# Kernel tuning notes

Hardware: AMD Instinct MI355X
Metric: run time of the kernel (lower is better)

Reference implementation:

```python
import jax, jax.numpy as jnp
import numpy as np

EPS = 1e-7
N_CAPS_J = 24
ROUTE_MIN = 0.0
N_ITER = 3
INV_TEMP = 0.5
INV_TEMP_DELTA = 0.1


def create_coords_mat(batch, d, h, w, ch, matrix_dim, rel_center=True):
    # Coordinate addition: pad (d,h,w) grid coords to matrix_dim (zeros first).
    subs = (d // 2, h // 2, w // 2) if rel_center else (0, 0, 0)
    f32 = jnp.float32
    dd = jnp.broadcast_to(jnp.arange(d, dtype=f32).reshape(d, 1, 1, 1, 1), (d, h, w, ch, 1)) - subs[0]
    hh = jnp.broadcast_to(jnp.arange(h, dtype=f32).reshape(1, h, 1, 1, 1), (d, h, w, ch, 1)) - subs[1]
    ww = jnp.broadcast_to(jnp.arange(w, dtype=f32).reshape(1, 1, w, 1, 1), (d, h, w, ch, 1)) - subs[2]
    c = jnp.concatenate([dd, hh, ww], -1).reshape(1, d * h * w, ch, 3)
    c = jnp.broadcast_to(c, (batch, d * h * w, ch, 3))
    zeros = jnp.zeros((batch, d * h * w, ch, matrix_dim - 3), dtype=f32)
    return jnp.concatenate([zeros, c], -1)  # (B, dhw, ch, matrix_dim)


def em_routing(v, a_i, beta_v, beta_a):
    # v: (B, Ci, Cj, M) votes; a_i: (B, Ci, 1) input activations.
    B, Ci, Cj, M = v.shape
    a_i = a_i[..., None]  # (B, Ci, 1, 1)

    def stats(r):
        den = r.sum(1, keepdims=True) + EPS                                   # (B,1,Cj,1)
        m = (v * r).sum(1, keepdims=True) / (den + EPS)                       # (B,1,Cj,M)
        s = (r * jnp.square(v - m)).sum(1, keepdims=True) / (den + EPS)       # (B,1,Cj,M)
        cost = ((beta_v + jnp.log(jnp.sqrt(s + EPS) + EPS)) * den).sum(-1, keepdims=True)  # (B,1,Cj,1)
        cm = cost.mean(-2, keepdims=True)
        cs = jnp.sqrt(jnp.square(cost - cm).sum(-2, keepdims=True) / Cj + EPS)
        return m, s, cost, cm, cs

    # Initialization step (uniform assignment scaled by input activations).
    r0 = jnp.full((B, Ci, Cj, 1), 1.0 / Cj, dtype=v.dtype) * a_i
    m, s, cost, cm, cs = stats(r0)
    a_j = jax.nn.sigmoid(INV_TEMP * (beta_a + (cm - cost) / (cs + EPS)))      # (B,1,Cj,1)

    def route(carry, counter):
        mean, stdsqr, act_j, it = carry
        # E-step: Gaussian log-likelihood of each vote under each output capsule.
        expo = (jnp.square(v - mean) / (2.0 * stdsqr + EPS)).sum(-1)          # (B,Ci,Cj)
        coef = -0.5 * jnp.log(2.0 * np.pi * stdsqr + EPS).sum(-1)             # (B,1,Cj)
        log_ap = jnp.log(act_j + EPS).reshape(B, 1, Cj) + coef - expo
        r_ij = jax.nn.softmax(log_ap + EPS, axis=-1)[..., None] * a_i         # (B,Ci,Cj,1)
        # M-step
        m, s, cost, cm, cs = stats(r_ij)
        it = it + counter * INV_TEMP_DELTA
        act = jax.nn.sigmoid(it * (beta_a + (cm - cost) / (cs + EPS)))
        return (m, s, act, it), None

    counters = jnp.arange(1, N_ITER, dtype=v.dtype)  # while_loop runs for counter=1..n_iterations-1
    init = (m, s, a_j, jnp.asarray(INV_TEMP, v.dtype))
    (mean, _, act_j, _), _ = jax.lax.scan(route, init, counters)
    return mean.reshape(B, Cj, M), act_j.reshape(B, Cj, 1)


def setup_inputs() -> dict:
    key = jax.random.key(0)
    k1, k2, k3, k4, k5 = jax.random.split(key, 5)
    B, D, H, W, Ch, M = 4, 4, 14, 14, 32, 16
    J = N_CAPS_J
    pose = jax.random.normal(k1, (B, D, H, W, Ch, M), dtype=jnp.float32)
    activation = jax.random.uniform(k2, (B, D, H, W, Ch, 1), dtype=jnp.float32)
    w = 0.1 * jax.random.normal(k3, (Ch, J, 4, 4), dtype=jnp.float32)
    beta_v = 0.1 * jax.random.normal(k4, (J, M), dtype=jnp.float32)
    beta_a = 0.1 * jax.random.normal(k5, (J, 1), dtype=jnp.float32)
    return {"pose": pose, "activation": activation, "w": w, "beta_v": beta_v, "beta_a": beta_a}


def reference(pose, activation, w, beta_v, beta_a):
    B, D, H, W, Ch, M = pose.shape
    n_i = D * H * W
    sq = int(np.sqrt(M))  # 4x4 pose matrices
    u = pose.reshape(B, n_i, Ch, sq, sq)
    coords = create_coords_mat(B, D, H, W, Ch, M, rel_center=True)            # (B,n_i,Ch,M)
    # Votes: each 4x4 pose matrix times per-(channel, out-capsule) transform.
    votes = jnp.einsum('bicpk,cjkq->bicjpq', u, w).reshape(B, n_i, Ch, N_CAPS_J, M)
    votes = votes + coords[:, :, :, None, :]  # coordinate addition (broadcast over Cj)
    votes = votes.reshape(B, n_i * Ch, N_CAPS_J, M)
    acts = activation.reshape(B, n_i * Ch, 1)
    acts = jnp.where(acts >= ROUTE_MIN, acts, 0.0)
    return em_routing(votes, acts, beta_v, beta_a)
```

## Files before the change

kernel.cpp:

```cpp
#include <hip/hip_runtime.h>
#include <math.h>

#define EPS 1e-7f
#define JC 24
#define CHN 32
#define D_ 4
#define H_ 14
#define W_ 14
#define NI 784
#define CI 25088
#define BATCH 4
#define NP 792
#define ST_STRIDE 792
#define NR2 16
#define TWO_PI 6.28318530717958647692f
#define LOG2E 1.44269504088896340736f

__device__ __forceinline__ float groupReduceSum16(float x) {
    x += __shfl_xor(x, 1);
    x += __shfl_xor(x, 2);
    x += __shfl_xor(x, 4);
    x += __shfl_xor(x, 8);
    return x;
}

template<int CTRL>
__device__ __forceinline__ float dpp_mv(float x) {
    return __int_as_float(__builtin_amdgcn_update_dpp(
        0, __float_as_int(x), CTRL, 0xF, 0xF, true));
}

__device__ __forceinline__ float groupSum32_dpp(float x) {
    x += dpp_mv<0xB1>(x);
    x += dpp_mv<0x4E>(x);
    x += dpp_mv<0x141>(x);
    x += dpp_mv<0x140>(x);
    x += __shfl_xor(x, 16);
    return x;
}

template<int PASS, int SPB, int CSEG>
__global__ __launch_bounds__(256, 3)
void accum_kernel(const float* __restrict__ pose, const float* __restrict__ act,
                  const float* __restrict__ w, const float* __restrict__ ST,
                  float* __restrict__ P) {
    __shared__ float w_lds[CSEG * 16 * JC];
    __shared__ float red[4 * JC * 33];

    const int t = threadIdx.x;
    const int h = t >> 5;
    const int jl = t & 31;
    const int jc = jl < 23 ? jl : 23;
    const int b = blockIdx.z;
    const int c0 = blockIdx.y * CSEG;
    const int sp0 = blockIdx.x * SPB;

    for (int idx = t; idx < CSEG * 384; idx += 256) {
        const int cs = idx / 384;
        const int r2 = idx - cs * 384;
        const int jj = r2 >> 4;
        const int kq = r2 & 15;
        const int k2 = kq >> 1, q2 = kq & 1;
        w_lds[((cs * 8 + k2) * JC + jj) * 2 + q2] =
            w[((size_t)(c0 + cs) * JC + jj) * 16 + kq];
    }

    float SA[16], MS[16], K = 0.f;
    if (PASS) {
        const float* stb = ST + b * ST_STRIDE;
        #pragma unroll
        for (int m4 = 0; m4 < 4; ++m4) {
            float4 a4 = *(const float4*)&stb[jc * 16 + m4 * 4];
            SA[m4*4+0] = a4.x; SA[m4*4+1] = a4.y; SA[m4*4+2] = a4.z; SA[m4*4+3] = a4.w;
            float4 b4 = *(const float4*)&stb[384 + jc * 16 + m4 * 4];
            MS[m4*4+0] = b4.x; MS[m4*4+1] = b4.y; MS[m4*4+2] = b4.z; MS[m4*4+3] = b4.w;
        }
        K = stb[768 + jc];
    }

    float accR = 0.f, accV[16], accV2[16];
    #pragma unroll
    for (int m = 0; m < 16; ++m) { accV[m] = 0.f; accV2[m] = 0.f; }

    __syncthreads();

    #pragma unroll 1
    for (int r = 0; r < SPB / 8; ++r) {
        const int sp = sp0 + r * 8 + h;
        const int dd = sp / (H_ * W_);
        const int rem = sp - dd * (H_ * W_);
        const int hh = rem / W_;
        const int ww = rem - hh * W_;
        const float cd = (float)(dd - D_ / 2);
        const float ch = (float)(hh - H_ / 2);
        const float cw = (float)(ww - W_ / 2);

        const float* upb = pose + (((size_t)b * NI + sp) * CHN + c0) * 16;
        const float* apb = act + ((size_t)b * NI + sp) * CHN + c0;

        float4 pu0 = *(const float4*)(upb + 0);
        float4 pu1 = *(const float4*)(upb + 4);
        float4 pu2 = *(const float4*)(upb + 8);
        float4 pu3 = *(const float4*)(upb + 12);
        float pa = apb[0];

        #pragma unroll 2
        for (int cs = 0; cs < CSEG; ++cs) {
            float4 uu[4] = { pu0, pu1, pu2, pu3 };
            float a = fmaxf(pa, 0.f);

            {
                const int nc = (cs + 1 < CSEG) ? cs + 1 : CSEG - 1;
                const float* upn = upb + nc * 16;
                pu0 = *(const float4*)(upn + 0);
                pu1 = *(const float4*)(upn + 4);
                pu2 = *(const float4*)(upn + 8);
                pu3 = *(const float4*)(upn + 12);
                pa = apb[nc];
            }

            float wv[16];
            #pragma unroll
            for (int k2 = 0; k2 < 8; ++k2) {
                float2 t2 = *(const float2*)&w_lds[((cs * 8 + k2) * JC + jc) * 2];
                wv[k2 * 2 + 0] = t2.x;
                wv[k2 * 2 + 1] = t2.y;
            }

            float v[16];
            #pragma unroll
            for (int p = 0; p < 4; ++p) {
                const float4 u = uu[p];
                #pragma unroll
                for (int q = 0; q < 4; ++q) {
                    v[p*4+q] = fmaf(u.w, wv[12+q],
                               fmaf(u.z, wv[8+q],
                               fmaf(u.y, wv[4+q], u.x * wv[q])));
                }
            }
            v[13] += cd; v[14] += ch; v[15] += cw;

            float rr;
            if (PASS) {
                float ex0 = 0.f, ex1 = 0.f, ex2 = 0.f, ex3 = 0.f;
                #pragma unroll
                for (int m4 = 0; m4 < 4; ++m4) {
                    float d0 = fmaf(v[m4*4+0], SA[m4*4+0], -MS[m4*4+0]);
                    float d1 = fmaf(v[m4*4+1], SA[m4*4+1], -MS[m4*4+1]);
                    float d2 = fmaf(v[m4*4+2], SA[m4*4+2], -MS[m4*4+2]);
                    float d3 = fmaf(v[m4*4+3], SA[m4*4+3], -MS[m4*4+3]);
                    ex0 = fmaf(d0, d0, ex0);
                    ex1 = fmaf(d1, d1, ex1);
                    ex2 = fmaf(d2, d2, ex2);
                    ex3 = fmaf(d3, d3, ex3);
                }
                float expo = (ex0 + ex1) + (ex2 + ex3);
                float e = (jl < JC) ? exp2f(K - expo) : 0.f;
                float S = groupSum32_dpp(e) + 1e-30f;
                rr = e * a * __frcp_rn(S);
            } else {
                rr = a * (1.0f / 24.0f);
            }

            accR += rr;
            #pragma unroll
            for (int m = 0; m < 16; ++m) {
                accV[m]  = fmaf(rr, v[m], accV[m]);
                accV2[m] = fmaf(rr, v[m] * v[m], accV2[m]);
            }
        }
    }

    accR += __shfl_xor(accR, 32);
    #pragma unroll
    for (int m = 0; m < 16; ++m) {
        accV[m]  += __shfl_xor(accV[m], 32);
        accV2[m] += __shfl_xor(accV2[m], 32);
    }
    const int wid = t >> 6;
    if ((t & 63) < JC) {
        float* rp = &red[(wid * JC + (t & 63)) * 33];
        #pragma unroll
        for (int m = 0; m < 16; ++m) { rp[m] = accV[m]; rp[16 + m] = accV2[m]; }
        rp[32] = accR;
    }
    __syncthreads();

    const int nblkTot = gridDim.x * gridDim.y;
    const int pidx = blockIdx.y * gridDim.x + blockIdx.x;
    for (int idx = t; idx < NP; idx += 256) {
        int j, v;
        if (idx < 384)      { j = idx >> 4;        v = idx & 15; }
        else if (idx < 768) { j = (idx-384) >> 4;  v = 16 + ((idx-384) & 15); }
        else                { j = idx - 768;       v = 32; }
        int o = (j * 33) + v;
        float s = red[o] + red[792 + o] + red[2*792 + o] + red[3*792 + o];
        P[((size_t)b * NP + idx) * nblkTot + pidx] = s;
    }
}

__global__ __launch_bounds__(256)
void reduce_kernel(const float* __restrict__ P, float* __restrict__ P2,
                   int nblk) {
    const int b = blockIdx.y;
    const int t = threadIdx.x;
    const int idx = blockIdx.x * 16 + (t >> 4);
    const int r = t & 15;
    if (idx >= NP) return;
    const int chunk = (nblk + NR2 - 1) / NR2;
    const int b0 = r * chunk;
    const int b1 = min(b0 + chunk, nblk);
    const float* p = P + ((size_t)b * NP + idx) * nblk;
    float s = 0.f;
    for (int k = b0; k < b1; ++k) s += p[k];
    P2[((size_t)b * NP + idx) * NR2 + r] = s;
}

__global__ __launch_bounds__(384)
void stats_kernel(const float* __restrict__ P2, const float* __restrict__ beta_v,
                  const float* __restrict__ beta_a, float* __restrict__ ST,
                  float* __restrict__ out, float it, int final_) {
    __shared__ float red[8];
    const int t = threadIdx.x;
    const int j = t >> 4, m = t & 15;
    const int b = blockIdx.x;
    const int wid = t >> 6, lane = t & 63;

    const float* pb = P2 + (size_t)b * NP * NR2;
    const float* p1 = pb + (size_t)t * NR2;
    const float* p2 = pb + (size_t)(384 + t) * NR2;
    const float* p3 = pb + (size_t)(768 + j) * NR2;
    float S1 = 0.f, S2 = 0.f, R = 0.f;
    #pragma unroll
    for (int r4 = 0; r4 < NR2; r4 += 4) {
        float4 a = *(const float4*)(p1 + r4);
        S1 += (a.x + a.y) + (a.z + a.w);
        float4 c = *(const float4*)(p2 + r4);
        S2 += (c.x + c.y) + (c.z + c.w);
        float4 d = *(const float4*)(p3 + r4);
        R += (d.x + d.y) + (d.z + d.w);
    }

    float den  = R + EPS;
    float denp = den + EPS;
    float mean = S1 / denp;
    float s = (S2 - 2.f * mean * S1 + mean * mean * R) / denp;
    s = fmaxf(s, 0.f);

    float c1 = beta_v[j * 16 + m] + logf(sqrtf(s + EPS) + EPS);
    float sc = groupReduceSum16(c1);
    float cost = den * sc;

    float t4 = cost + __shfl_xor(cost, 16);
    t4 += __shfl_xor(t4, 32);
    __syncthreads();
    if (lane == 0) red[wid] = t4;
    __syncthreads();
    float tot = red[0] + red[1] + red[2] + red[3] + red[4] + red[5];
    float cm = tot / 24.f;

    float d2 = cost - cm; d2 *= d2;
    float t4b = d2 + __shfl_xor(d2, 16);
    t4b += __shfl_xor(t4b, 32);
    __syncthreads();
    if (lane == 0) red[wid] = t4b;
    __syncthreads();
    float tot2 = red[0] + red[1] + red[2] + red[3] + red[4] + red[5];
    float cs = sqrtf(tot2 / 24.f + EPS);

    float x = it * (beta_a[j] + (cm - cost) / (cs + EPS));
    float aj = 1.f / (1.f + expf(-x));

    float coef = -0.5f * groupReduceSum16(logf(TWO_PI * s + EPS));

    float Aq = LOG2E / (2.f * s + EPS);
    float SAq = sqrtf(Aq);

    float* stb = ST + b * ST_STRIDE;
    stb[t]       = SAq;
    stb[384 + t] = mean * SAq;
    if (m == 0) stb[768 + j] = (logf(aj + EPS) + coef) * LOG2E;

    if (final_) {
        out[(b * 24 + j) * 16 + m] = mean;
        if (m == 0) out[1536 + b * 24 + j] = aj;
    }
}

template<int SPB, int CSEG>
static void run_all(int spblk, int cblk,
                    const float* pose, const float* act, const float* w,
                    const float* beta_v, const float* beta_a,
                    float* P, float* P2, float* ST, float* out,
                    hipStream_t stream) {
    dim3 agrid(spblk, cblk, BATCH), ablock(256);
    dim3 rgrid((NP + 15) / 16, BATCH), rblock(256);
    dim3 sgrid(BATCH), sblock(384);
    const int nblk = spblk * cblk;

    accum_kernel<0, SPB, CSEG><<<agrid, ablock, 0, stream>>>(pose, act, w, ST, P);
    reduce_kernel<<<rgrid, rblock, 0, stream>>>(P, P2, nblk);
    stats_kernel<<<sgrid, sblock, 0, stream>>>(P2, beta_v, beta_a, ST, out, 0.5f, 0);

    accum_kernel<1, SPB, CSEG><<<agrid, ablock, 0, stream>>>(pose, act, w, ST, P);
    reduce_kernel<<<rgrid, rblock, 0, stream>>>(P, P2, nblk);
    stats_kernel<<<sgrid, sblock, 0, stream>>>(P2, beta_v, beta_a, ST, out, 0.6f, 0);

    accum_kernel<1, SPB, CSEG><<<agrid, ablock, 0, stream>>>(pose, act, w, ST, P);
    reduce_kernel<<<rgrid, rblock, 0, stream>>>(P, P2, nblk);
    stats_kernel<<<sgrid, sblock, 0, stream>>>(P2, beta_v, beta_a, ST, out, 0.8f, 1);
}

extern "C" void kernel_launch(void* const* d_in, const int* in_sizes, int n_in,
                              void* d_out, int out_size, void* d_ws, size_t ws_size,
                              hipStream_t stream) {
    const float* pose   = (const float*)d_in[0];
    const float* act    = (const float*)d_in[1];
    const float* w      = (const float*)d_in[2];
    const float* beta_v = (const float*)d_in[3];
    const float* beta_a = (const float*)d_in[4];
    float* out = (float*)d_out;
    float* W   = (float*)d_ws;

    const size_t p2_elems = (size_t)BATCH * NP * NR2;
    const size_t st_elems = (size_t)BATCH * ST_STRIDE;
    auto need = [&](int spblk, int cblk) -> size_t {
        return ((size_t)BATCH * NP * spblk * cblk + p2_elems + st_elems) * 4;
    };

    if (need(98, 2) <= ws_size) {
        float* P  = W;
        float* P2 = W + (size_t)BATCH * NP * 98 * 2;
        float* ST = P2 + p2_elems;
        run_all<8, 16>(98, 2, pose, act, w, beta_v, beta_a, P, P2, ST, out, stream);
    } else if (need(49, 1) <= ws_size) {
        float* P  = W;
        float* P2 = W + (size_t)BATCH * NP * 49;
        float* ST = P2 + p2_elems;
        run_all<16, 32>(49, 1, pose, act, w, beta_v, beta_a, P, P2, ST, out, stream);
    } else {
        float* P  = W;
        float* P2 = W + (size_t)BATCH * NP * 7;
        float* ST = P2 + p2_elems;
        run_all<112, 32>(7, 1, pose, act, w, beta_v, beta_a, P, P2, ST, out, stream);
    }
}
```

Baseline: 100.3 us.

## Process two spatial positions per thread sharing LDS weight loads

Each thread now handles two spatial positions per outer iteration, reusing one set of transform weights read from LDS for both vote computations and interleaving their independent pose prefetches. The primary configuration also changes from 98 spatial x 2 channel blocks to 49 spatial x 4 channel blocks (SPB 16, CSEG 8). The aim is to halve LDS weight traffic per vote and add instruction-level parallelism. In exchange it raises register pressure, with two sets of pose registers alongside the 32 accumulators, under launch bounds of 3 blocks, which may cause spills or lower occupancy.

```diff
diff --git a/kernel.cpp b/kernel.cpp
--- a/kernel.cpp
+++ b/kernel.cpp
@@ -39,6 +39,70 @@
     return x;
 }
 
+template<int PASS>
+__device__ __forceinline__ void vote_step(
+    float4& pu0, float4& pu1, float4& pu2, float4& pu3, float& pa,
+    const float* upb, const float* apb, int nc,
+    const float* wv, float cd, float ch, float cw,
+    const float* SA, const float* MS, float K, int jl,
+    float& accR, float* accV, float* accV2) {
+
+    const float4 u0 = pu0, u1 = pu1, u2 = pu2, u3 = pu3;
+    const float a = fmaxf(pa, 0.f);
+
+    {
+        const float* upn = upb + nc * 16;
+        pu0 = *(const float4*)(upn + 0);
+        pu1 = *(const float4*)(upn + 4);
+        pu2 = *(const float4*)(upn + 8);
+        pu3 = *(const float4*)(upn + 12);
+        pa = apb[nc];
+    }
+
+    float v[16];
+    #pragma unroll
+    for (int q = 0; q < 4; ++q) {
+        v[0*4+q] = fmaf(u0.w, wv[12+q], fmaf(u0.z, wv[8+q],
+                   fmaf(u0.y, wv[4+q], u0.x * wv[q])));
+        v[1*4+q] = fmaf(u1.w, wv[12+q], fmaf(u1.z, wv[8+q],
+                   fmaf(u1.y, wv[4+q], u1.x * wv[q])));
+        v[2*4+q] = fmaf(u2.w, wv[12+q], fmaf(u2.z, wv[8+q],
+                   fmaf(u2.y, wv[4+q], u2.x * wv[q])));
+        v[3*4+q] = fmaf(u3.w, wv[12+q], fmaf(u3.z, wv[8+q],
+                   fmaf(u3.y, wv[4+q], u3.x * wv[q])));
+    }
+    v[13] += cd; v[14] += ch; v[15] += cw;
+
+    float rr;
+    if (PASS) {
+        float ex0 = 0.f, ex1 = 0.f, ex2 = 0.f, ex3 = 0.f;
+        #pragma unroll
+        for (int m4 = 0; m4 < 4; ++m4) {
+            float d0 = fmaf(v[m4*4+0], SA[m4*4+0], -MS[m4*4+0]);
+            float d1 = fmaf(v[m4*4+1], SA[m4*4+1], -MS[m4*4+1]);
+            float d2 = fmaf(v[m4*4+2], SA[m4*4+2], -MS[m4*4+2]);
+            float d3 = fmaf(v[m4*4+3], SA[m4*4+3], -MS[m4*4+3]);
+            ex0 = fmaf(d0, d0, ex0);
+            ex1 = fmaf(d1, d1, ex1);
+            ex2 = fmaf(d2, d2, ex2);
+            ex3 = fmaf(d3, d3, ex3);
+        }
+        float expo = (ex0 + ex1) + (ex2 + ex3);
+        float e = (jl < JC) ? exp2f(K - expo) : 0.f;
+        float S = groupSum32_dpp(e) + 1e-30f;
+        rr = e * a * __frcp_rn(S);
+    } else {
+        rr = a * (1.0f / 24.0f);
+    }
+
+    accR += rr;
+    #pragma unroll
+    for (int m = 0; m < 16; ++m) {
+        accV[m]  = fmaf(rr, v[m], accV[m]);
+        accV2[m] = fmaf(rr, v[m] * v[m], accV2[m]);
+    }
+}
+
 template<int PASS, int SPB, int CSEG>
 __global__ __launch_bounds__(256, 3)
 void accum_kernel(const float* __restrict__ pose, const float* __restrict__ act,
@@ -85,40 +149,44 @@
     __syncthreads();
 
     #pragma unroll 1
-    for (int r = 0; r < SPB / 8; ++r) {
-        const int sp = sp0 + r * 8 + h;
-        const int dd = sp / (H_ * W_);
-        const int rem = sp - dd * (H_ * W_);
-        const int hh = rem / W_;
-        const int ww = rem - hh * W_;
-        const float cd = (float)(dd - D_ / 2);
-        const float ch = (float)(hh - H_ / 2);
-        const float cw = (float)(ww - W_ / 2);
-
-        const float* upb = pose + (((size_t)b * NI + sp) * CHN + c0) * 16;
-        const float* apb = act + ((size_t)b * NI + sp) * CHN + c0;
-
-        float4 pu0 = *(const float4*)(upb + 0);
-        float4 pu1 = *(const float4*)(upb + 4);
-        float4 pu2 = *(const float4*)(upb + 8);
-        float4 pu3 = *(const float4*)(upb + 12);
-        float pa = apb[0];
-
-        #pragma unroll 2
+    for (int r = 0; r < SPB / 16; ++r) {
+        const int spA = sp0 + r * 16 + h;
+        const int spB = spA + 8;
+
+        int ddA = spA / (H_ * W_);
+        int remA = spA - ddA * (H_ * W_);
+        int hhA = remA / W_;
+        int wwA = remA - hhA * W_;
+        const float cdA = (float)(ddA - D_ / 2);
+        const float chA = (float)(hhA - H_ / 2);
+        const float cwA = (float)(wwA - W_ / 2);
+
+        int ddB = spB / (H_ * W_);
+        int remB = spB - ddB * (H_ * W_);
+        int hhB = remB / W_;
+        int wwB = remB - hhB * W_;
+        const float cdB = (float)(ddB - D_ / 2);
+        const float chB = (float)(hhB - H_ / 2);
+        const float cwB = (float)(wwB - W_ / 2);
+
+        const float* upbA = pose + (((size_t)b * NI + spA) * CHN + c0) * 16;
+        const float* apbA = act + ((size_t)b * NI + spA) * CHN + c0;
+        const float* upbB = pose + (((size_t)b * NI + spB) * CHN + c0) * 16;
+        const float* apbB = act + ((size_t)b * NI + spB) * CHN + c0;
+
+        float4 puA0 = *(const float4*)(upbA + 0);
+        float4 puA1 = *(const float4*)(upbA + 4);
+        float4 puA2 = *(const float4*)(upbA + 8);
+        float4 puA3 = *(const float4*)(upbA + 12);
+        float paA = apbA[0];
+        float4 puB0 = *(const float4*)(upbB + 0);
+        float4 puB1 = *(const float4*)(upbB + 4);
+        float4 puB2 = *(const float4*)(upbB + 8);
+        float4 puB3 = *(const float4*)(upbB + 12);
+        float paB = apbB[0];
+
+        #pragma unroll 1
         for (int cs = 0; cs < CSEG; ++cs) {
-            float4 uu[4] = { pu0, pu1, pu2, pu3 };
-            float a = fmaxf(pa, 0.f);
-
-            {
-                const int nc = (cs + 1 < CSEG) ? cs + 1 : CSEG - 1;
-                const float* upn = upb + nc * 16;
-                pu0 = *(const float4*)(upn + 0);
-                pu1 = *(const float4*)(upn + 4);
-                pu2 = *(const float4*)(upn + 8);
-                pu3 = *(const float4*)(upn + 12);
-                pa = apb[nc];
-            }
-
             float wv[16];
             #pragma unroll
             for (int k2 = 0; k2 < 8; ++k2) {
@@ -126,48 +194,14 @@
                 wv[k2 * 2 + 0] = t2.x;
                 wv[k2 * 2 + 1] = t2.y;
             }
-
-            float v[16];
-            #pragma unroll
-            for (int p = 0; p < 4; ++p) {
-                const float4 u = uu[p];
-                #pragma unroll
-                for (int q = 0; q < 4; ++q) {
-                    v[p*4+q] = fmaf(u.w, wv[12+q],
-                               fmaf(u.z, wv[8+q],
-                               fmaf(u.y, wv[4+q], u.x * wv[q])));
-                }
-            }
-            v[13] += cd; v[14] += ch; v[15] += cw;
-
-            float rr;
-            if (PASS) {
-                float ex0 = 0.f, ex1 = 0.f, ex2 = 0.f, ex3 = 0.f;
-                #pragma unroll
-                for (int m4 = 0; m4 < 4; ++m4) {
-                    float d0 = fmaf(v[m4*4+0], SA[m4*4+0], -MS[m4*4+0]);
-                    float d1 = fmaf(v[m4*4+1], SA[m4*4+1], -MS[m4*4+1]);
-                    float d2 = fmaf(v[m4*4+2], SA[m4*4+2], -MS[m4*4+2]);
-                    float d3 = fmaf(v[m4*4+3], SA[m4*4+3], -MS[m4*4+3]);
-                    ex0 = fmaf(d0, d0, ex0);
-                    ex1 = fmaf(d1, d1, ex1);
-                    ex2 = fmaf(d2, d2, ex2);
-                    ex3 = fmaf(d3, d3, ex3);
-                }
-                float expo = (ex0 + ex1) + (ex2 + ex3);
-                float e = (jl < JC) ? exp2f(K - expo) : 0.f;
-                float S = groupSum32_dpp(e) + 1e-30f;
-                rr = e * a * __frcp_rn(S);
-            } else {
-                rr = a * (1.0f / 24.0f);
-            }
-
-            accR += rr;
-            #pragma unroll
-            for (int m = 0; m < 16; ++m) {
-                accV[m]  = fmaf(rr, v[m], accV[m]);
-                accV2[m] = fmaf(rr, v[m] * v[m], accV2[m]);
-            }
+            const int nc = (cs + 1 < CSEG) ? cs + 1 : CSEG - 1;
+
+            vote_step<PASS>(puA0, puA1, puA2, puA3, paA, upbA, apbA, nc,
+                            wv, cdA, chA, cwA, SA, MS, K, jl,
+                            accR, accV, accV2);
+            vote_step<PASS>(puB0, puB1, puB2, puB3, paB, upbB, apbB, nc,
+                            wv, cdB, chB, cwB, SA, MS, K, jl,
+                            accR, accV, accV2);
         }
     }
 
@@ -328,11 +362,11 @@
         return ((size_t)BATCH * NP * spblk * cblk + p2_elems + st_elems) * 4;
     };
 
-    if (need(98, 2) <= ws_size) {
+    if (need(49, 4) <= ws_size) {
         float* P  = W;
-        float* P2 = W + (size_t)BATCH * NP * 98 * 2;
+        float* P2 = W + (size_t)BATCH * NP * 49 * 4;
         float* ST = P2 + p2_elems;
-        run_all<8, 16>(98, 2, pose, act, w, beta_v, beta_a, P, P2, ST, out, stream);
+        run_all<16, 8>(49, 4, pose, act, w, beta_v, beta_a, P, P2, ST, out, stream);
     } else if (need(49, 1) <= ws_size) {
         float* P  = W;
         float* P2 = W + (size_t)BATCH * NP * 49;
```

Result: no change. 99.04 us, median of 2 (-1.2%).
